# Optimization experiments

Measured on AMD Instinct MI355X. Metric: run time of the kernel, lower is better.

The kernel has to match this reference:

```python
import jax, jax.numpy as jnp
import numpy as np

B, H, S, D = 1, 16, 2048, 64


def setup_inputs() -> dict:
    key = jax.random.key(0)
    kq, kk, kv, km = jax.random.split(key, 4)
    q = jax.random.normal(kq, (B, H, S, D), dtype=jnp.float32)
    k = jax.random.normal(kk, (B, H, S, D), dtype=jnp.float32)
    v = jax.random.normal(kv, (B, H, S, D), dtype=jnp.float32)
    omask = jax.random.uniform(km, (B, H, S, S), dtype=jnp.float32)
    return {"q": q, "k": k, "v": v, "omask": omask}


def reference(q, k, v, omask):
    # mask = omask / sqrt(rowsum(omask)), nan -> 0
    row_sum = jnp.sum(omask, axis=-1, keepdims=True)  # [B,H,S,1]
    decay_mask = jnp.nan_to_num(omask / jnp.sqrt(row_sum), nan=0.0)
    # retention = (q k^T) * mask  -> [B,H,S,S]
    retention = jnp.einsum("bhsd,bhtd->bhst", q, k) * decay_mask
    # normalize by |rowsum(retention)| clamped to >= 1 (detached in original)
    scale = jnp.clip(jnp.abs(jnp.sum(retention, axis=-1, keepdims=True)), 1.0, None)
    retention = retention / scale
    # output = retention @ v -> [B,H,S,D]
    return jnp.einsum("bhst,bhtd->bhsd", retention, v)
```

## Files before the change

kernel.cpp:

```cpp
#include <hip/hip_runtime.h>

#define H 16
#define S 2048
#define D 64
#define BM 64
#define BN 64
#define NT (S / BN)
#define KP 72

typedef __attribute__((ext_vector_type(8))) short bf16x8;
typedef __attribute__((ext_vector_type(4))) short short4v;
typedef __attribute__((ext_vector_type(4))) float fx4;

static __device__ __forceinline__ short f2bf(float x) {
    unsigned u = __float_as_uint(x);
    u += 0x7fffu + ((u >> 16) & 1u);
    return (short)(u >> 16);
}
static __device__ __forceinline__ float bf2f(short s) {
    return __uint_as_float(((unsigned)(unsigned short)s) << 16);
}

__global__ __launch_bounds__(256)
void ParallelRetention_origin_25374666785438_kernel(
    const float* __restrict__ q, const float* __restrict__ k,
    const float* __restrict__ v, const float* __restrict__ om,
    float* __restrict__ out)
{
    __shared__ short ldsKh[2][BN * KP];
    __shared__ short ldsKl[2][BN * KP];
    __shared__ short ldsVT[2][BN * KP];
    __shared__ short ldsP[4 * 16 * KP];

    const int tid  = threadIdx.x;
    const int wave = tid >> 6;
    const int lane = tid & 63;
    const int col  = lane & 15;
    const int quad = lane >> 4;
    const int t_base = (tid >> 4) << 2;
    const int d4     = (tid & 15) << 2;

    const int h  = blockIdx.x & 15;
    const int qb = blockIdx.x >> 4;
    const int row0 = qb * BM;

    const size_t headQK = (size_t)h * S * D;
    const size_t headM  = (size_t)h * S * S;

    bf16x8 qh[2], qlo[2];
    {
        const int s_row = row0 + wave * 16 + col;
        const float* qp = q + headQK + (size_t)s_row * D + quad * 8;
#pragma unroll
        for (int c = 0; c < 2; ++c) {
            fx4 a = *(const fx4*)(qp + c * 32);
            fx4 b = *(const fx4*)(qp + c * 32 + 4);
            float f[8] = {a[0],a[1],a[2],a[3],b[0],b[1],b[2],b[3]};
#pragma unroll
            for (int j = 0; j < 8; ++j) {
                short hi = f2bf(f[j]);
                qh[c][j]  = hi;
                qlo[c][j] = f2bf(f[j] - bf2f(hi));
            }
        }
    }

    fx4 U[4];
#pragma unroll
    for (int nt = 0; nt < 4; ++nt) { U[nt][0]=0.f; U[nt][1]=0.f; U[nt][2]=0.f; U[nt][3]=0.f; }
    float rs_acc[4] = {0.f, 0.f, 0.f, 0.f};
    float T_acc[4]  = {0.f, 0.f, 0.f, 0.f};
    float om0[16], om1[16];

    const float* kbase0 = k + headQK;
    const float* vbase0 = v + headQK;
    const float* ombase = om + headM + (size_t)(row0 + wave * 16) * S;

    auto load_kv = [&](int t0, fx4 (&kr)[4], fx4 (&vr)[4]) {
        const float* kb = kbase0 + (size_t)t0 * D;
        const float* vb = vbase0 + (size_t)t0 * D;
#pragma unroll
        for (int r = 0; r < 4; ++r) {
            kr[r] = *(const fx4*)(kb + (size_t)(t_base + r) * D + d4);
            vr[r] = *(const fx4*)(vb + (size_t)(t_base + r) * D + d4);
        }
    };
    auto load_om = [&](int t0, float (&o)[16]) {
        const float* omp = ombase + t0;
#pragma unroll
        for (int tn = 0; tn < 4; ++tn)
#pragma unroll
            for (int r = 0; r < 4; ++r)
                o[tn * 4 + r] = omp[(size_t)(quad * 4 + r) * S + tn * 16 + col];
    };
    auto stage_write = [&](const fx4 (&kr)[4], const fx4 (&vr)[4],
                           short* Kh, short* Kl, short* VT) {
#pragma unroll
        for (int r = 0; r < 4; ++r) {
            short4v h4, l4;
#pragma unroll
            for (int j = 0; j < 4; ++j) {
                short hi = f2bf(kr[r][j]);
                h4[j] = hi;
                l4[j] = f2bf(kr[r][j] - bf2f(hi));
            }
            *(short4v*)(&Kh[(t_base + r) * KP + d4]) = h4;
            *(short4v*)(&Kl[(t_base + r) * KP + d4]) = l4;
        }
#pragma unroll
        for (int j = 0; j < 4; ++j) {
            short4v p;
#pragma unroll
            for (int r = 0; r < 4; ++r) p[r] = f2bf(vr[r][j]);
            *(short4v*)(&VT[(d4 + j) * KP + t_base]) = p;
        }
    };
    auto compute = [&](const short* Kh, const short* Kl, const short* VT,
                       const float (&omc)[16]) {
#pragma unroll
        for (int tn = 0; tn < 4; ++tn) {
            const short* kph = &Kh[(tn * 16 + col) * KP + quad * 8];
            const short* kpl = &Kl[(tn * 16 + col) * KP + quad * 8];
            bf16x8 kh0 = *(const bf16x8*)(kph);
            bf16x8 kh1 = *(const bf16x8*)(kph + 32);
            bf16x8 kl0 = *(const bf16x8*)(kpl);
            bf16x8 kl1 = *(const bf16x8*)(kpl + 32);
            fx4 z; z[0]=0.f; z[1]=0.f; z[2]=0.f; z[3]=0.f;
            z = __builtin_amdgcn_mfma_f32_16x16x32_bf16(qh[0],  kh0, z, 0, 0, 0);
            z = __builtin_amdgcn_mfma_f32_16x16x32_bf16(qh[1],  kh1, z, 0, 0, 0);
            z = __builtin_amdgcn_mfma_f32_16x16x32_bf16(qh[0],  kl0, z, 0, 0, 0);
            z = __builtin_amdgcn_mfma_f32_16x16x32_bf16(qh[1],  kl1, z, 0, 0, 0);
            z = __builtin_amdgcn_mfma_f32_16x16x32_bf16(qlo[0], kh0, z, 0, 0, 0);
            z = __builtin_amdgcn_mfma_f32_16x16x32_bf16(qlo[1], kh1, z, 0, 0, 0);
#pragma unroll
            for (int r = 0; r < 4; ++r) {
                float m = omc[tn * 4 + r];
                float p = z[r] * m;
                rs_acc[r] += m;
                T_acc[r]  += p;
                ldsP[(wave * 16 + quad * 4 + r) * KP + tn * 16 + col] = f2bf(p);
            }
        }
#pragma unroll
        for (int kt = 0; kt < 2; ++kt) {
            bf16x8 pa = *(const bf16x8*)(&ldsP[(wave * 16 + col) * KP + kt * 32 + quad * 8]);
#pragma unroll
            for (int nt = 0; nt < 4; ++nt) {
                bf16x8 vb = *(const bf16x8*)(&VT[(nt * 16 + col) * KP + kt * 32 + quad * 8]);
                U[nt] = __builtin_amdgcn_mfma_f32_16x16x32_bf16(pa, vb, U[nt], 0, 0, 0);
            }
        }
    };

    {
        fx4 kr[4], vr[4];
        load_kv(0, kr, vr);
        load_om(0, om0);
        stage_write(kr, vr, ldsKh[0], ldsKl[0], ldsVT[0]);
    }

    for (int it2 = 0; it2 < NT; it2 += 2) {
        {
            __syncthreads();
            fx4 kr[4], vr[4];
            load_kv((it2 + 1) * BN, kr, vr);
            load_om((it2 + 1) * BN, om1);
            compute(ldsKh[0], ldsKl[0], ldsVT[0], om0);
            stage_write(kr, vr, ldsKh[1], ldsKl[1], ldsVT[1]);
        }
        {
            __syncthreads();
            const bool pf = (it2 + 2 < NT);
            fx4 kr[4], vr[4];
            if (pf) {
                load_kv((it2 + 2) * BN, kr, vr);
                load_om((it2 + 2) * BN, om0);
            }
            compute(ldsKh[1], ldsKl[1], ldsVT[1], om1);
            if (pf) stage_write(kr, vr, ldsKh[0], ldsKl[0], ldsVT[0]);
        }
    }

#pragma unroll
    for (int off = 1; off < 16; off <<= 1) {
#pragma unroll
        for (int r = 0; r < 4; ++r) {
            rs_acc[r] += __shfl_xor(rs_acc[r], off, 64);
            T_acc[r]  += __shfl_xor(T_acc[r], off, 64);
        }
    }
    float factor[4];
#pragma unroll
    for (int r = 0; r < 4; ++r) {
        float rs  = rs_acc[r];
        float inv = rs > 0.f ? rsqrtf(rs) : 0.f;
        float rowsum = T_acc[r] * inv;
        float sc = fabsf(rowsum);
        sc = sc < 1.f ? 1.f : sc;
        factor[r] = inv / sc;
    }
    float* op = out + headQK + (size_t)(row0 + wave * 16) * D;
#pragma unroll
    for (int r = 0; r < 4; ++r)
#pragma unroll
        for (int nt = 0; nt < 4; ++nt)
            op[(size_t)(quad * 4 + r) * D + nt * 16 + col] = U[nt][r] * factor[r];
}

extern "C" void kernel_launch(void* const* d_in, const int* in_sizes, int n_in,
                              void* d_out, int out_size, void* d_ws, size_t ws_size,
                              hipStream_t stream) {
    const float* q  = (const float*)d_in[0];
    const float* k  = (const float*)d_in[1];
    const float* v  = (const float*)d_in[2];
    const float* om = (const float*)d_in[3];
    float* out = (float*)d_out;
    (void)in_sizes; (void)n_in; (void)out_size; (void)d_ws; (void)ws_size;

    dim3 grid(H * (S / BM));
    dim3 block(256);
    hipLaunchKernelGGL(ParallelRetention_origin_25374666785438_kernel,
                       grid, block, 0, stream, q, k, v, om, out);
}
```

Before: 407.1 us.

## Use XOR-swizzled fragment-major LDS layout and packed bf16 conversion

```diff
diff --git a/kernel.cpp b/kernel.cpp
--- a/kernel.cpp
+++ b/kernel.cpp
@@ -1,4 +1,5 @@
 #include <hip/hip_runtime.h>
+#include <hip/hip_bf16.h>
 
 #define H 16
 #define S 2048
@@ -6,11 +7,11 @@
 #define BM 64
 #define BN 64
 #define NT (S / BN)
-#define KP 72
 
 typedef __attribute__((ext_vector_type(8))) short bf16x8;
-typedef __attribute__((ext_vector_type(4))) short short4v;
 typedef __attribute__((ext_vector_type(4))) float fx4;
+typedef __attribute__((ext_vector_type(4))) unsigned uintx4;
+typedef __attribute__((ext_vector_type(2))) unsigned uintx2;
 
 static __device__ __forceinline__ short f2bf(float x) {
     unsigned u = __float_as_uint(x);
@@ -20,6 +21,12 @@
 static __device__ __forceinline__ float bf2f(short s) {
     return __uint_as_float(((unsigned)(unsigned short)s) << 16);
 }
+static __device__ __forceinline__ unsigned pkbf(float a, float b) {
+    union { __hip_bfloat162 h; unsigned u; } c;
+    c.h = __float22bfloat162_rn(make_float2(a, b));
+    return c.u;
+}
+
 
 __global__ __launch_bounds__(256)
 void ParallelRetention_origin_25374666785438_kernel(
@@ -27,18 +34,41 @@
     const float* __restrict__ v, const float* __restrict__ om,
     float* __restrict__ out)
 {
-    __shared__ short ldsKh[2][BN * KP];
-    __shared__ short ldsKl[2][BN * KP];
-    __shared__ short ldsVT[2][BN * KP];
-    __shared__ short ldsP[4 * 16 * KP];
+    __shared__ __align__(16) short ldsKh[2][4096];
+    __shared__ __align__(16) short ldsKl[2][4096];
+    __shared__ __align__(16) short ldsVT[2][4096];
+    __shared__ __align__(16) short ldsP[4096];
 
     const int tid  = threadIdx.x;
     const int wave = tid >> 6;
     const int lane = tid & 63;
     const int col  = lane & 15;
     const int quad = lane >> 4;
+    const int ls8  = (lane ^ ((lane >> 3) & 7)) << 3;
+
+    const int krow = tid >> 2;
+    const int ksub = tid & 3;
+    const int kfA  = ((krow >> 4) * 2 + (ksub >> 1)) * 64 + ((ksub & 1) * 2) * 16 + (krow & 15);
+    const int kwA  = (kfA ^ ((kfA >> 3) & 7)) << 3;
+    const int kfB  = kfA + 16;
+    const int kwB  = (kfB ^ ((kfB >> 3) & 7)) << 3;
+
     const int t_base = (tid >> 4) << 2;
     const int d4     = (tid & 15) << 2;
+    int vtw[4];
+#pragma unroll
+    for (int dd = 0; dd < 4; ++dd) {
+        int d = d4 + dd;
+        int f = ((d >> 4) * 2 + (t_base >> 5)) * 64 + ((t_base >> 3) & 3) * 16 + (d & 15);
+        vtw[dd] = ((f ^ ((f >> 3) & 7)) << 3) + (t_base & 7);
+    }
+
+    const int Cc = ((col >> 3) << 1) + (quad >> 1);
+    int C8[4];
+#pragma unroll
+    for (int r = 0; r < 4; ++r) C8[r] = (r ^ Cc) << 3;
+    const int pbase = wave * 1024 + (col >> 3) * 128 + quad * 32 + (col & 7);
+    const int pb0 = pbase, pb1 = pbase ^ 32;
 
     const int h  = blockIdx.x & 15;
     const int qb = blockIdx.x >> 4;
@@ -77,13 +107,12 @@
     const float* ombase = om + headM + (size_t)(row0 + wave * 16) * S;
 
     auto load_kv = [&](int t0, fx4 (&kr)[4], fx4 (&vr)[4]) {
-        const float* kb = kbase0 + (size_t)t0 * D;
+        const float* kb = kbase0 + (size_t)t0 * D + (size_t)krow * D + ksub * 16;
         const float* vb = vbase0 + (size_t)t0 * D;
 #pragma unroll
-        for (int r = 0; r < 4; ++r) {
-            kr[r] = *(const fx4*)(kb + (size_t)(t_base + r) * D + d4);
-            vr[r] = *(const fx4*)(vb + (size_t)(t_base + r) * D + d4);
-        }
+        for (int i = 0; i < 4; ++i) kr[i] = *(const fx4*)(kb + i * 4);
+#pragma unroll
+        for (int r = 0; r < 4; ++r) vr[r] = *(const fx4*)(vb + (size_t)(t_base + r) * D + d4);
     };
     auto load_om = [&](int t0, float (&o)[16]) {
         const float* omp = ombase + t0;
@@ -93,38 +122,43 @@
             for (int r = 0; r < 4; ++r)
                 o[tn * 4 + r] = omp[(size_t)(quad * 4 + r) * S + tn * 16 + col];
     };
-    auto stage_write = [&](const fx4 (&kr)[4], const fx4 (&vr)[4],
-                           short* Kh, short* Kl, short* VT) {
-#pragma unroll
-        for (int r = 0; r < 4; ++r) {
-            short4v h4, l4;
-#pragma unroll
-            for (int j = 0; j < 4; ++j) {
-                short hi = f2bf(kr[r][j]);
-                h4[j] = hi;
-                l4[j] = f2bf(kr[r][j] - bf2f(hi));
-            }
-            *(short4v*)(&Kh[(t_base + r) * KP + d4]) = h4;
-            *(short4v*)(&Kl[(t_base + r) * KP + d4]) = l4;
-        }
-#pragma unroll
-        for (int j = 0; j < 4; ++j) {
-            short4v p;
-#pragma unroll
-            for (int r = 0; r < 4; ++r) p[r] = f2bf(vr[r][j]);
-            *(short4v*)(&VT[(d4 + j) * KP + t_base]) = p;
-        }
-    };
-    auto compute = [&](const short* Kh, const short* Kl, const short* VT,
-                       const float (&omc)[16]) {
+    auto stage_write = [&](const fx4 (&kr)[4], const fx4 (&vr)[4], int buf) {
+        float kf[16];
+#pragma unroll
+        for (int i = 0; i < 4; ++i) {
+            kf[i*4+0]=kr[i][0]; kf[i*4+1]=kr[i][1]; kf[i*4+2]=kr[i][2]; kf[i*4+3]=kr[i][3];
+        }
+        unsigned hh[8], ll[8];
+#pragma unroll
+        for (int p = 0; p < 8; ++p) {
+            float a = kf[2*p], b = kf[2*p+1];
+            unsigned u = pkbf(a, b);
+            hh[p] = u;
+            float la = a - __uint_as_float(u << 16);
+            float lb = b - __uint_as_float(u & 0xffff0000u);
+            ll[p] = pkbf(la, lb);
+        }
+        *(uintx4*)(&ldsKh[buf][kwA]) = uintx4{hh[0], hh[1], hh[2], hh[3]};
+        *(uintx4*)(&ldsKh[buf][kwB]) = uintx4{hh[4], hh[5], hh[6], hh[7]};
+        *(uintx4*)(&ldsKl[buf][kwA]) = uintx4{ll[0], ll[1], ll[2], ll[3]};
+        *(uintx4*)(&ldsKl[buf][kwB]) = uintx4{ll[4], ll[5], ll[6], ll[7]};
+#pragma unroll
+        for (int dd = 0; dd < 4; ++dd) {
+            unsigned p0 = pkbf(vr[0][dd], vr[1][dd]);
+            unsigned p1 = pkbf(vr[2][dd], vr[3][dd]);
+            *(uintx2*)(&ldsVT[buf][vtw[dd]]) = uintx2{p0, p1};
+        }
+    };
+    auto compute = [&](int buf, const float (&omc)[16]) {
+        const short* Kh = ldsKh[buf];
+        const short* Kl = ldsKl[buf];
+        const short* VT = ldsVT[buf];
 #pragma unroll
         for (int tn = 0; tn < 4; ++tn) {
-            const short* kph = &Kh[(tn * 16 + col) * KP + quad * 8];
-            const short* kpl = &Kl[(tn * 16 + col) * KP + quad * 8];
-            bf16x8 kh0 = *(const bf16x8*)(kph);
-            bf16x8 kh1 = *(const bf16x8*)(kph + 32);
-            bf16x8 kl0 = *(const bf16x8*)(kpl);
-            bf16x8 kl1 = *(const bf16x8*)(kpl + 32);
+            bf16x8 kh0 = *(const bf16x8*)(&Kh[(tn*2+0)*512 + ls8]);
+            bf16x8 kh1 = *(const bf16x8*)(&Kh[(tn*2+1)*512 + ls8]);
+            bf16x8 kl0 = *(const bf16x8*)(&Kl[(tn*2+0)*512 + ls8]);
+            bf16x8 kl1 = *(const bf16x8*)(&Kl[(tn*2+1)*512 + ls8]);
             fx4 z; z[0]=0.f; z[1]=0.f; z[2]=0.f; z[3]=0.f;
             z = __builtin_amdgcn_mfma_f32_16x16x32_bf16(qh[0],  kh0, z, 0, 0, 0);
             z = __builtin_amdgcn_mfma_f32_16x16x32_bf16(qh[1],  kh1, z, 0, 0, 0);
@@ -132,22 +166,23 @@
             z = __builtin_amdgcn_mfma_f32_16x16x32_bf16(qh[1],  kl1, z, 0, 0, 0);
             z = __builtin_amdgcn_mfma_f32_16x16x32_bf16(qlo[0], kh0, z, 0, 0, 0);
             z = __builtin_amdgcn_mfma_f32_16x16x32_bf16(qlo[1], kh1, z, 0, 0, 0);
+            const int pa = ((tn & 1) ? pb1 : pb0) + (tn >> 1) * 512 + (tn & 1) * 256;
 #pragma unroll
             for (int r = 0; r < 4; ++r) {
                 float m = omc[tn * 4 + r];
                 float p = z[r] * m;
                 rs_acc[r] += m;
                 T_acc[r]  += p;
-                ldsP[(wave * 16 + quad * 4 + r) * KP + tn * 16 + col] = f2bf(p);
+                ldsP[pa + C8[r]] = f2bf(p);
             }
         }
 #pragma unroll
         for (int kt = 0; kt < 2; ++kt) {
-            bf16x8 pa = *(const bf16x8*)(&ldsP[(wave * 16 + col) * KP + kt * 32 + quad * 8]);
+            bf16x8 paf = *(const bf16x8*)(&ldsP[wave*1024 + kt*512 + ls8]);
 #pragma unroll
             for (int nt = 0; nt < 4; ++nt) {
-                bf16x8 vb = *(const bf16x8*)(&VT[(nt * 16 + col) * KP + kt * 32 + quad * 8]);
-                U[nt] = __builtin_amdgcn_mfma_f32_16x16x32_bf16(pa, vb, U[nt], 0, 0, 0);
+                bf16x8 vb = *(const bf16x8*)(&VT[(nt*2+kt)*512 + ls8]);
+                U[nt] = __builtin_amdgcn_mfma_f32_16x16x32_bf16(paf, vb, U[nt], 0, 0, 0);
             }
         }
     };
@@ -156,7 +191,7 @@
         fx4 kr[4], vr[4];
         load_kv(0, kr, vr);
         load_om(0, om0);
-        stage_write(kr, vr, ldsKh[0], ldsKl[0], ldsVT[0]);
+        stage_write(kr, vr, 0);
     }
 
     for (int it2 = 0; it2 < NT; it2 += 2) {
@@ -165,8 +200,8 @@
             fx4 kr[4], vr[4];
             load_kv((it2 + 1) * BN, kr, vr);
             load_om((it2 + 1) * BN, om1);
-            compute(ldsKh[0], ldsKl[0], ldsVT[0], om0);
-            stage_write(kr, vr, ldsKh[1], ldsKl[1], ldsVT[1]);
+            compute(0, om0);
+            stage_write(kr, vr, 1);
         }
         {
             __syncthreads();
@@ -176,8 +211,8 @@
                 load_kv((it2 + 2) * BN, kr, vr);
                 load_om((it2 + 2) * BN, om0);
             }
-            compute(ldsKh[1], ldsKl[1], ldsVT[1], om1);
-            if (pf) stage_write(kr, vr, ldsKh[0], ldsKl[0], ldsVT[0]);
+            compute(1, om1);
+            if (pf) stage_write(kr, vr, 0);
         }
     }
 
```

After: 411.4 us. Within noise of the previous version (+1.1%).
